# Kernel tuning notes

Measured on AMD Instinct MI355X. Metric: run time of the kernel, lower is better.

The kernel has to match this reference:

```python
import jax, jax.numpy as jnp
import numpy as np
import math

B, S, HID, H, D = 8, 1024, 1024, 16, 64
MAX_POS = 1024  # max_position_embeddings


def setup_inputs() -> dict:
    key = jax.random.key(0)
    ks = jax.random.split(key, 8)
    sc = 1.0 / math.sqrt(HID)
    return {
        "hidden_states": jax.random.normal(ks[0], (B, S, HID), jnp.float32),
        "Wq": jax.random.normal(ks[1], (HID, HID), jnp.float32) * sc,
        "bq": jnp.zeros((HID,), jnp.float32),
        "Wk": jax.random.normal(ks[2], (HID, HID), jnp.float32) * sc,
        "bk": jnp.zeros((HID,), jnp.float32),
        "Wv": jax.random.normal(ks[3], (HID, HID), jnp.float32) * sc,
        "bv": jnp.zeros((HID,), jnp.float32),
        "dist_table": jax.random.normal(ks[4], (2 * MAX_POS - 1, D), jnp.float32) * 0.02,
    }


def _heads(x):
    # [B,S,HID] -> [B,H,S,D]
    return x.reshape(B, S, H, D).transpose(0, 2, 1, 3)


def reference(hidden_states, Wq, bq, Wk, bk, Wv, bv, dist_table):
    q = _heads(hidden_states @ Wq + bq)            # [B,H,S,D]
    k = _heads(hidden_states @ Wk + bk)            # [B,H,S,D]
    # NOTE: source bug — value_layer uses the key projection in self-attention path.
    v = _heads(hidden_states @ Wk + bk)            # [B,H,S,D]

    scores = jnp.einsum("bhld,bhrd->bhlr", q, k)   # [B,H,S,S]

    # relative_key_query positional bias
    pos = jnp.arange(S)
    distance = pos[:, None] - pos[None, :]          # [S,S] in [-(S-1), S-1]
    pos_emb = dist_table[distance + MAX_POS - 1]    # [S,S,D]
    rel_q = jnp.einsum("bhld,lrd->bhlr", q, pos_emb)
    rel_k = jnp.einsum("bhrd,lrd->bhlr", k, pos_emb)
    scores = (scores + rel_q + rel_k) / math.sqrt(D)

    probs = jax.nn.softmax(scores, axis=-1)         # dropout is identity at inference
    ctx = jnp.einsum("bhlr,bhrd->bhld", probs, v)   # [B,H,S,D]
    ctx = ctx.transpose(0, 2, 1, 3).reshape(B, S, HID)
    return ctx
```

## Files before the change

### kernel.cpp

```cpp
#include <hip/hip_runtime.h>
#include <hip/hip_bf16.h>


typedef float  f32x4 __attribute__((ext_vector_type(4)));
typedef short  s16x8 __attribute__((ext_vector_type(8)));
typedef unsigned short u16x4 __attribute__((ext_vector_type(4)));

#define MFMA16(a,b,c) __builtin_amdgcn_mfma_f32_16x16x32_bf16((a),(b),(c),0,0,0)

static __device__ __forceinline__ unsigned short f2b(float x){
    unsigned int u = __float_as_uint(x);
    unsigned int r = (u + 0x7fffu + ((u >> 16) & 1u)) >> 16;
    return (unsigned short)r;
}
static __device__ __forceinline__ float b2f(unsigned short b){
    return __uint_as_float(((unsigned int)b) << 16);
}
static __device__ __forceinline__ void gl_lds16(const unsigned short* g, unsigned short* l){
    __builtin_amdgcn_global_load_lds(
        (const __attribute__((address_space(1))) unsigned int*)g,
        (__attribute__((address_space(3))) unsigned int*)l, 16, 0, 0);
}

__global__ void prep_table(const float* __restrict__ T, unsigned short* __restrict__ Tb){
    int i = blockIdx.x * 256 + threadIdx.x;
    if (i < 2047 * 64)      Tb[i] = f2b(T[i]);
    else if (i < 2048 * 64) Tb[i] = 0;
}

__global__ __launch_bounds__(256)
void prep_a(const float* __restrict__ Hs,
            unsigned short* __restrict__ Ahi, unsigned short* __restrict__ Alo){
    int i = (blockIdx.x * 256 + threadIdx.x) * 8;
    float v[8];
    *(f32x4*)&v[0] = *(const f32x4*)(Hs + i);
    *(f32x4*)&v[4] = *(const f32x4*)(Hs + i + 4);
    unsigned short h8[8] __attribute__((aligned(16)));
    unsigned short l8[8] __attribute__((aligned(16)));
#pragma unroll
    for (int j = 0; j < 8; j++) {
        unsigned short h = f2b(v[j]);
        h8[j] = h;
        l8[j] = f2b(v[j] - b2f(h));
    }
    *(s16x8*)&Ahi[i] = *(s16x8*)h8;
    *(s16x8*)&Alo[i] = *(s16x8*)l8;
}

__global__ __launch_bounds__(256)
void prep_w(const float* __restrict__ Wq, const float* __restrict__ Wk,
            unsigned short* __restrict__ WqThi, unsigned short* __restrict__ WqTlo,
            unsigned short* __restrict__ WkThi, unsigned short* __restrict__ WkTlo){
    __shared__ unsigned short LH[64][72];
    __shared__ unsigned short LL[64][72];
    const int bx = blockIdx.x;
    const float* W = (bx & 1) ? Wk : Wq;
    unsigned short* Thi = (bx & 1) ? WkThi : WqThi;
    unsigned short* Tlo = (bx & 1) ? WkTlo : WqTlo;
    const int tile = bx >> 1;
    const int k0 = (tile >> 4) * 64, n0 = (tile & 15) * 64;
    const int t = threadIdx.x;
    const int r = t >> 3, c8 = (t & 7) * 8;
#pragma unroll
    for (int half = 0; half < 2; half++) {
        int rr = r + half * 32;
        const float* p = W + (size_t)(k0 + rr) * 1024 + n0 + c8;
        float v[8];
        *(f32x4*)&v[0] = *(const f32x4*)p;
        *(f32x4*)&v[4] = *(const f32x4*)(p + 4);
#pragma unroll
        for (int j = 0; j < 8; j++) {
            unsigned short h = f2b(v[j]);
            LH[rr][c8 + j] = h;
            LL[rr][c8 + j] = f2b(v[j] - b2f(h));
        }
    }
    __syncthreads();
    const int n = t >> 2, kg = (t & 3) * 16;
    unsigned short oh[16] __attribute__((aligned(16)));
    unsigned short ol[16] __attribute__((aligned(16)));
#pragma unroll
    for (int j = 0; j < 16; j++) { oh[j] = LH[kg + j][n]; ol[j] = LL[kg + j][n]; }
    unsigned short* dh = Thi + (size_t)(n0 + n) * 1024 + k0 + kg;
    unsigned short* dl = Tlo + (size_t)(n0 + n) * 1024 + k0 + kg;
    *(s16x8*)dh       = *(s16x8*)&oh[0];
    *(s16x8*)(dh + 8) = *(s16x8*)&oh[8];
    *(s16x8*)dl       = *(s16x8*)&ol[0];
    *(s16x8*)(dl + 8) = *(s16x8*)&ol[8];
}

__global__ __launch_bounds__(512, 4)
void proj_gemm(const unsigned short* __restrict__ Ahi, const unsigned short* __restrict__ Alo,
               const unsigned short* __restrict__ WqThi, const unsigned short* __restrict__ WqTlo,
               const unsigned short* __restrict__ WkThi, const unsigned short* __restrict__ WkTlo,
               const float* __restrict__ bq, const float* __restrict__ bk,
               unsigned short* __restrict__ qbf, unsigned short* __restrict__ kbf,
               unsigned short* __restrict__ kTbf)
{
    __shared__ __attribute__((aligned(16))) unsigned short SL[16384];

    const int t = threadIdx.x, lane = t & 63, w = t >> 6;
    const int q4 = lane >> 4, l15 = lane & 15;
    const int wm = w >> 1, wn = w & 1;
    const int ntile = blockIdx.x & 15, mtile = blockIdx.x >> 4;
    const int m0 = mtile * 128, cn0 = (ntile & 7) * 128;
    const unsigned short* Bh = (ntile < 8) ? WqThi : WkThi;
    const unsigned short* Bl = (ntile < 8) ? WqTlo : WkTlo;

    f32x4 acc[2][4];
#pragma unroll
    for (int i = 0; i < 2; i++)
#pragma unroll
        for (int j = 0; j < 4; j++) acc[i][j] = (f32x4){0.f, 0.f, 0.f, 0.f};

    const int lr = lane >> 2, lc = (lane & 3) * 8;

    for (int kk0 = 0; kk0 < 1024; kk0 += 32) {
        __syncthreads();
#pragma unroll
        for (int i = 0; i < 4; i++) {
            const int seg = w * 4 + i;
            const int tid = seg >> 3, row0 = (seg & 7) * 16;
            const unsigned short* g;
            if      (tid == 0) g = Ahi + (size_t)(m0 + row0 + lr) * 1024 + kk0 + lc;
            else if (tid == 1) g = Alo + (size_t)(m0 + row0 + lr) * 1024 + kk0 + lc;
            else if (tid == 2) g = Bh  + (size_t)(cn0 + row0 + lr) * 1024 + kk0 + lc;
            else               g = Bl  + (size_t)(cn0 + row0 + lr) * 1024 + kk0 + lc;
            gl_lds16(g, &SL[seg * 512]);
        }
        __syncthreads();

        s16x8 ah[2], al[2], bh8[4], bl8[4];
#pragma unroll
        for (int sm = 0; sm < 2; sm++) {
            int r = wm * 32 + sm * 16 + l15;
            ah[sm] = *(const s16x8*)&SL[r * 32 + q4 * 8];
            al[sm] = *(const s16x8*)&SL[4096 + r * 32 + q4 * 8];
        }
#pragma unroll
        for (int sn = 0; sn < 4; sn++) {
            int r = wn * 64 + sn * 16 + l15;
            bh8[sn] = *(const s16x8*)&SL[8192 + r * 32 + q4 * 8];
            bl8[sn] = *(const s16x8*)&SL[12288 + r * 32 + q4 * 8];
        }
#pragma unroll
        for (int sm = 0; sm < 2; sm++)
#pragma unroll
            for (int sn = 0; sn < 4; sn++) {
                f32x4 a = acc[sm][sn];
                a = MFMA16(ah[sm], bh8[sn], a);
                a = MFMA16(ah[sm], bl8[sn], a);
                a = MFMA16(al[sm], bh8[sn], a);
                acc[sm][sn] = a;
            }
    }

#pragma unroll
    for (int sm = 0; sm < 2; sm++) {
#pragma unroll
        for (int sn = 0; sn < 4; sn++) {
            const int coln = ntile * 128 + wn * 64 + sn * 16 + l15;
            const float bias = (ntile < 8) ? bq[coln] : bk[coln - 1024];
            const int mbase = m0 + wm * 32 + sm * 16 + q4 * 4;
            const int bb = mbase >> 10, ss0 = mbase & 1023;
            unsigned short vb[4];
#pragma unroll
            for (int reg = 0; reg < 4; reg++) vb[reg] = f2b(acc[sm][sn][reg] + bias);
            if (ntile < 8) {
                const int hh = coln >> 6, d = coln & 63;
#pragma unroll
                for (int reg = 0; reg < 4; reg++)
                    qbf[(((size_t)(bb * 16 + hh) * 1024) + ss0 + reg) * 64 + d] = vb[reg];
            } else {
                const int ck = coln - 1024;
                const int hh = ck >> 6, d = ck & 63;
#pragma unroll
                for (int reg = 0; reg < 4; reg++)
                    kbf[(((size_t)(bb * 16 + hh) * 1024) + ss0 + reg) * 64 + d] = vb[reg];
                u16x4 pk = { vb[0], vb[1], vb[2], vb[3] };
                *(u16x4*)&kTbf[(((size_t)(bb * 16 + hh) * 64) + d) * 1024 + ss0] = pk;
            }
        }
    }
}

__global__ __launch_bounds__(512, 4)
void attn(const unsigned short* __restrict__ qbf, const unsigned short* __restrict__ kbf,
          const unsigned short* __restrict__ kTbf, const unsigned short* __restrict__ Tbf,
          float* __restrict__ out)
{
    __shared__ __attribute__((aligned(16))) unsigned char LDSRAW[65536];
    unsigned short* Klds = (unsigned short*)LDSRAW;
    unsigned short* Tlds = (unsigned short*)(LDSRAW + 8192);
    unsigned int*   GqS  = (unsigned int*)(LDSRAW + 32768);
    unsigned short* Pw   = (unsigned short*)(LDSRAW + 49152);
    float*          Ep   = (float*)LDSRAW;

    const int t = threadIdx.x;
    const int lane = t & 63, w = t >> 6;
    const int q4 = lane >> 4, l15 = lane & 15;
    const int swz8 = (l15 & 7) * 8;
    const int bh = blockIdx.x & 127;
    const int lb = (blockIdx.x >> 7) * 128;
    const int l0w = lb + w * 16;

    const unsigned short* qb = qbf + (size_t)bh * 65536;
    const unsigned short* kb = kbf + (size_t)bh * 65536;
    const unsigned short* kT = kTbf + (size_t)bh * 65536;

    const s16x8 qf0 = *(const s16x8*)(qb + (l0w + l15) * 64 + q4 * 8);
    const s16x8 qf1 = *(const s16x8*)(qb + (l0w + l15) * 64 + 32 + q4 * 8);

    f32x4 pacc[4];
#pragma unroll
    for (int n = 0; n < 4; n++) pacc[n] = (f32x4){0.f, 0.f, 0.f, 0.f};
    float psum = 0.f;

    unsigned int*   GqW = GqS + w * 512;
    unsigned short* PwW = Pw + w * 1024;

    const int s_row = t >> 3;
    const int s_c8  = (t & 7) * 8;
    const int s_swc = s_c8 ^ ((s_row & 7) << 3);

    int r0 = 0;
    int lo = lb + 960;
    s16x8 kv  = *(const s16x8*)(kb + (size_t)(r0 + s_row) * 64 + s_c8);
    s16x8 tv0 = *(const s16x8*)(Tbf + (size_t)(lo + s_row) * 64 + s_c8);
    s16x8 tv1 = *(const s16x8*)(Tbf + (size_t)(lo + s_row + 64) * 64 + s_c8);
    s16x8 tv2 = *(const s16x8*)(Tbf + (size_t)(lo + s_row + 128) * 64 + s_c8);

    for (int c = 0; c < 16; c++) {
        __syncthreads();
        *(s16x8*)&Klds[s_row * 64 + s_swc]         = kv;
        *(s16x8*)&Tlds[s_row * 64 + s_swc]         = tv0;
        *(s16x8*)&Tlds[(s_row + 64) * 64 + s_swc]  = tv1;
        *(s16x8*)&Tlds[(s_row + 128) * 64 + s_swc] = tv2;
        __syncthreads();

        if (c < 15) {
            int r0n = r0 + 64, lon = lo - 64;
            kv  = *(const s16x8*)(kb + (size_t)(r0n + s_row) * 64 + s_c8);
            tv0 = *(const s16x8*)(Tbf + (size_t)(lon + s_row) * 64 + s_c8);
            tv1 = *(const s16x8*)(Tbf + (size_t)(lon + s_row + 64) * 64 + s_c8);
            tv2 = *(const s16x8*)(Tbf + (size_t)(lon + s_row + 128) * 64 + s_c8);
        }

#pragma unroll
        for (int rs = 0; rs < 4; rs++) {
            const int krow = rs * 16 + l15;
            const s16x8 kf0 = *(const s16x8*)&Klds[krow * 64 + ((q4 * 8) ^ swz8)];
            const s16x8 kf1 = *(const s16x8*)&Klds[krow * 64 + ((32 + q4 * 8) ^ swz8)];
            const int c0 = w * 16 - rs * 16 + 48;
            const int j0 = (c0 + l15) * 64, j1 = (c0 + 16 + l15) * 64;
            const s16x8 tf00 = *(const s16x8*)&Tlds[j0 + ((q4 * 8) ^ swz8)];
            const s16x8 tf01 = *(const s16x8*)&Tlds[j0 + ((32 + q4 * 8) ^ swz8)];
            const s16x8 tf10 = *(const s16x8*)&Tlds[j1 + ((q4 * 8) ^ swz8)];
            const s16x8 tf11 = *(const s16x8*)&Tlds[j1 + ((32 + q4 * 8) ^ swz8)];

            f32x4 s = (f32x4){0.f, 0.f, 0.f, 0.f};
            s = MFMA16(kf0, qf0, s);
            s = MFMA16(kf1, qf1, s);

            f32x4 gq0 = (f32x4){0.f,0.f,0.f,0.f}, gq1 = (f32x4){0.f,0.f,0.f,0.f};
            f32x4 hk0 = (f32x4){0.f,0.f,0.f,0.f}, hk1 = (f32x4){0.f,0.f,0.f,0.f};
            gq0 = MFMA16(qf0, tf00, gq0); gq0 = MFMA16(qf1, tf01, gq0);
            gq1 = MFMA16(qf0, tf10, gq1); gq1 = MFMA16(qf1, tf11, gq1);
            hk0 = MFMA16(kf0, tf00, hk0); hk0 = MFMA16(kf1, tf01, hk0);
            hk1 = MFMA16(kf0, tf10, hk1); hk1 = MFMA16(kf1, tf11, hk1);

            unsigned int* G = GqW + (rs & 1) * 256;
#pragma unroll
            for (int reg = 0; reg < 4; reg++) {
                unsigned int pk = (unsigned int)f2b(gq0[reg]) |
                                  ((unsigned int)f2b(gq1[reg]) << 16);
                G[(q4 * 4 + reg) * 16 + l15] = pk;
            }

            const int n4b = l15 - q4 * 4 + 15;
            float pr[4];
#pragma unroll
            for (int reg = 0; reg < 4; reg++) {
                const int n4 = n4b - reg;
                const int srclane = (n4 & 15) | (lane & 48);
                float a0 = __shfl(hk0[reg], srclane);
                float a1 = __shfl(hk1[reg], srclane);
                float relk = (n4 < 16) ? a0 : a1;
                unsigned int g = G[l15 * 16 + (n4 & 15)];
                float b0v = b2f((unsigned short)(g & 0xffffu));
                float b1v = b2f((unsigned short)(g >> 16));
                float relq = (n4 < 16) ? b0v : b1v;
                float sc = (s[reg] + relq + relk) * 0.125f - 4.0f;
                float p = __expf(sc);
                psum += p;
                pr[reg] = p;
            }
            unsigned int u0 = (unsigned int)f2b(pr[0]) | ((unsigned int)f2b(pr[1]) << 16);
            unsigned int u1 = (unsigned int)f2b(pr[2]) | ((unsigned int)f2b(pr[3]) << 16);
            unsigned long long pk2 = (unsigned long long)u0 | ((unsigned long long)u1 << 32);
            *(unsigned long long*)&PwW[l15 * 64 + ((rs * 16 + q4 * 4) ^ swz8)] = pk2;
        }

        const s16x8 pf0 = *(const s16x8*)&PwW[l15 * 64 + ((q4 * 8) ^ swz8)];
        const s16x8 pf1 = *(const s16x8*)&PwW[l15 * 64 + ((32 + q4 * 8) ^ swz8)];
#pragma unroll
        for (int n = 0; n < 4; n++) {
            const unsigned short* vp = kT + (size_t)(n * 16 + l15) * 1024 + r0;
            const s16x8 vf0 = *(const s16x8*)(vp + q4 * 8);
            const s16x8 vf1 = *(const s16x8*)(vp + 32 + q4 * 8);
            pacc[n] = MFMA16(vf0, pf0, pacc[n]);
            pacc[n] = MFMA16(vf1, pf1, pacc[n]);
        }

        r0 += 64;
        lo -= 64;
    }

    psum += __shfl_xor(psum, 16);
    psum += __shfl_xor(psum, 32);
    const float inv = 1.0f / psum;

    __syncthreads();
    float* EpW = Ep + w * 1088;
#pragma unroll
    for (int n = 0; n < 4; n++) {
        f32x4 v = pacc[n];
        v[0] *= inv; v[1] *= inv; v[2] *= inv; v[3] *= inv;
        *(f32x4*)&EpW[l15 * 68 + n * 16 + q4 * 4] = v;
    }
    const int b0 = bh >> 4, hh = bh & 15;
    const int li = lane >> 2, gg = lane & 3;
#pragma unroll
    for (int cc = 0; cc < 4; cc++) {
        f32x4 v = *(const f32x4*)&EpW[li * 68 + gg * 16 + cc * 4];
        *(f32x4*)&out[((size_t)(b0 * 1024 + l0w + li) * 1024) + hh * 64 + gg * 16 + cc * 4] = v;
    }
}

extern "C" void kernel_launch(void* const* d_in, const int* in_sizes, int n_in,
                              void* d_out, int out_size, void* d_ws, size_t ws_size,
                              hipStream_t stream) {
    (void)in_sizes; (void)n_in; (void)out_size; (void)ws_size;
    const float* Hs = (const float*)d_in[0];
    const float* Wq = (const float*)d_in[1];
    const float* bq = (const float*)d_in[2];
    const float* Wk = (const float*)d_in[3];
    const float* bk = (const float*)d_in[4];
    const float* Tt = (const float*)d_in[7];
    float* out = (float*)d_out;

    unsigned short* qbf   = (unsigned short*)d_ws;
    unsigned short* kbf   = qbf  + (size_t)8 * 1024 * 1024;
    unsigned short* kTbf  = kbf  + (size_t)8 * 1024 * 1024;
    unsigned short* Tbf   = kTbf + (size_t)8 * 1024 * 1024;
    unsigned short* Ahi   = Tbf  + (size_t)2048 * 64;
    unsigned short* Alo   = Ahi  + (size_t)8 * 1024 * 1024;
    unsigned short* WqThi = Alo  + (size_t)8 * 1024 * 1024;
    unsigned short* WqTlo = WqThi + (size_t)1024 * 1024;
    unsigned short* WkThi = WqTlo + (size_t)1024 * 1024;
    unsigned short* WkTlo = WkThi + (size_t)1024 * 1024;

    hipLaunchKernelGGL(prep_table, dim3(512), dim3(256), 0, stream, Tt, Tbf);
    hipLaunchKernelGGL(prep_a, dim3(4096), dim3(256), 0, stream, Hs, Ahi, Alo);
    hipLaunchKernelGGL(prep_w, dim3(512), dim3(256), 0, stream,
                       Wq, Wk, WqThi, WqTlo, WkThi, WkTlo);
    hipLaunchKernelGGL(proj_gemm, dim3(1024), dim3(512), 0, stream,
                       Ahi, Alo, WqThi, WqTlo, WkThi, WkTlo, bq, bk, qbf, kbf, kTbf);
    hipLaunchKernelGGL(attn, dim3(1024), dim3(512), 0, stream,
                       qbf, kbf, kTbf, Tbf, out);
}
```

Before: 411.3 us.

## Use ring-buffered table tiles, direct global-to-LDS loads, and packed bf16 conversions

The positional-table tile in LDS becomes a 192-row ring buffer. Each chunk loads only the 64 new table rows and the new K tile, using global_load_lds (direct global-to-LDS) instead of register staging, and one of the two table fragments is carried over from the previous rs step in registers. Value loads are issued at the top of each chunk to hide latency. The rel-q LDS staging is vectorised with a padded stride, the rel-k shuffle is halved by packing both halves into bf16 before shuffling, and conversions use the hardware packed bf16 instruction. This cuts global and LDS traffic and VALU work, but rel-k is now rounded to bf16 before it is added, and correctness depends on the global_load_lds layout matching the XOR swizzle.

```diff
diff --git a/kernel.cpp b/kernel.cpp
--- a/kernel.cpp
+++ b/kernel.cpp
@@ -5,6 +5,7 @@
 typedef float  f32x4 __attribute__((ext_vector_type(4)));
 typedef short  s16x8 __attribute__((ext_vector_type(8)));
 typedef unsigned short u16x4 __attribute__((ext_vector_type(4)));
+typedef unsigned int   u32x4 __attribute__((ext_vector_type(4)));
 
 #define MFMA16(a,b,c) __builtin_amdgcn_mfma_f32_16x16x32_bf16((a),(b),(c),0,0,0)
 
@@ -15,6 +16,15 @@
 }
 static __device__ __forceinline__ float b2f(unsigned short b){
     return __uint_as_float(((unsigned int)b) << 16);
+}
+static __device__ __forceinline__ unsigned int cvtpk(float a, float b){
+#if defined(__has_builtin) && __has_builtin(__builtin_amdgcn_cvt_pk_bf16_f32)
+    typedef __bf16 bf16x2_t __attribute__((ext_vector_type(2)));
+    bf16x2_t v = __builtin_amdgcn_cvt_pk_bf16_f32(a, b);
+    unsigned int u; __builtin_memcpy(&u, &v, 4); return u;
+#else
+    return (unsigned int)f2b(a) | ((unsigned int)f2b(b) << 16);
+#endif
 }
 static __device__ __forceinline__ void gl_lds16(const unsigned short* g, unsigned short* l){
     __builtin_amdgcn_global_load_lds(
@@ -189,11 +199,11 @@
           const unsigned short* __restrict__ kTbf, const unsigned short* __restrict__ Tbf,
           float* __restrict__ out)
 {
-    __shared__ __attribute__((aligned(16))) unsigned char LDSRAW[65536];
+    __shared__ __attribute__((aligned(16))) unsigned char LDSRAW[59392];
     unsigned short* Klds = (unsigned short*)LDSRAW;
     unsigned short* Tlds = (unsigned short*)(LDSRAW + 8192);
     unsigned int*   GqS  = (unsigned int*)(LDSRAW + 32768);
-    unsigned short* Pw   = (unsigned short*)(LDSRAW + 49152);
+    unsigned short* Pw   = (unsigned short*)(LDSRAW + 43008);
     float*          Ep   = (float*)LDSRAW;
 
     const int t = threadIdx.x;
@@ -211,52 +221,56 @@
     const s16x8 qf0 = *(const s16x8*)(qb + (l0w + l15) * 64 + q4 * 8);
     const s16x8 qf1 = *(const s16x8*)(qb + (l0w + l15) * 64 + 32 + q4 * 8);
 
+    const int dj_r = lane >> 3;
+    const int dj_c = ((lane & 7) ^ dj_r) * 8;
+
+#pragma unroll
+    for (int i = 0; i < 4; i++) {
+        const int seg = w * 4 + i;
+        if (seg < 24) {
+            const unsigned short* g = Tbf + (size_t)(lb + 960 + seg * 8 + dj_r) * 64 + dj_c;
+            gl_lds16(g, Tlds + seg * 512);
+        } else {
+            const int s = seg - 24;
+            const unsigned short* g = kb + (size_t)(s * 8 + dj_r) * 64 + dj_c;
+            gl_lds16(g, Klds + s * 512);
+        }
+    }
+    __syncthreads();
+
     f32x4 pacc[4];
 #pragma unroll
     for (int n = 0; n < 4; n++) pacc[n] = (f32x4){0.f, 0.f, 0.f, 0.f};
     float psum = 0.f;
 
-    unsigned int*   GqW = GqS + w * 512;
+    unsigned int*   GqW = GqS + w * 320;
     unsigned short* PwW = Pw + w * 1024;
 
-    const int s_row = t >> 3;
-    const int s_c8  = (t & 7) * 8;
-    const int s_swc = s_c8 ^ ((s_row & 7) << 3);
+    const int pB0 = 64 + w * 16 + l15;
+    s16x8 tb0 = *(const s16x8*)&Tlds[pB0 * 64 + ((q4 * 8) ^ swz8)];
+    s16x8 tb1 = *(const s16x8*)&Tlds[pB0 * 64 + ((32 + q4 * 8) ^ swz8)];
 
     int r0 = 0;
-    int lo = lb + 960;
-    s16x8 kv  = *(const s16x8*)(kb + (size_t)(r0 + s_row) * 64 + s_c8);
-    s16x8 tv0 = *(const s16x8*)(Tbf + (size_t)(lo + s_row) * 64 + s_c8);
-    s16x8 tv1 = *(const s16x8*)(Tbf + (size_t)(lo + s_row + 64) * 64 + s_c8);
-    s16x8 tv2 = *(const s16x8*)(Tbf + (size_t)(lo + s_row + 128) * 64 + s_c8);
-
     for (int c = 0; c < 16; c++) {
-        __syncthreads();
-        *(s16x8*)&Klds[s_row * 64 + s_swc]         = kv;
-        *(s16x8*)&Tlds[s_row * 64 + s_swc]         = tv0;
-        *(s16x8*)&Tlds[(s_row + 64) * 64 + s_swc]  = tv1;
-        *(s16x8*)&Tlds[(s_row + 128) * 64 + s_swc] = tv2;
-        __syncthreads();
-
-        if (c < 15) {
-            int r0n = r0 + 64, lon = lo - 64;
-            kv  = *(const s16x8*)(kb + (size_t)(r0n + s_row) * 64 + s_c8);
-            tv0 = *(const s16x8*)(Tbf + (size_t)(lon + s_row) * 64 + s_c8);
-            tv1 = *(const s16x8*)(Tbf + (size_t)(lon + s_row + 64) * 64 + s_c8);
-            tv2 = *(const s16x8*)(Tbf + (size_t)(lon + s_row + 128) * 64 + s_c8);
-        }
-
+        s16x8 vf[4][2];
+#pragma unroll
+        for (int n = 0; n < 4; n++) {
+            const unsigned short* vp = kT + (size_t)(n * 16 + l15) * 1024 + r0;
+            vf[n][0] = *(const s16x8*)(vp + q4 * 8);
+            vf[n][1] = *(const s16x8*)(vp + 32 + q4 * 8);
+        }
+
+        const int base = 1008 - 64 * c + w * 16;
 #pragma unroll
         for (int rs = 0; rs < 4; rs++) {
             const int krow = rs * 16 + l15;
             const s16x8 kf0 = *(const s16x8*)&Klds[krow * 64 + ((q4 * 8) ^ swz8)];
             const s16x8 kf1 = *(const s16x8*)&Klds[krow * 64 + ((32 + q4 * 8) ^ swz8)];
-            const int c0 = w * 16 - rs * 16 + 48;
-            const int j0 = (c0 + l15) * 64, j1 = (c0 + 16 + l15) * 64;
-            const s16x8 tf00 = *(const s16x8*)&Tlds[j0 + ((q4 * 8) ^ swz8)];
-            const s16x8 tf01 = *(const s16x8*)&Tlds[j0 + ((32 + q4 * 8) ^ swz8)];
-            const s16x8 tf10 = *(const s16x8*)&Tlds[j1 + ((q4 * 8) ^ swz8)];
-            const s16x8 tf11 = *(const s16x8*)&Tlds[j1 + ((32 + q4 * 8) ^ swz8)];
+
+            const int p0 = (base - rs * 16) % 192;
+            int pa = p0 + l15; if (pa >= 192) pa -= 192;
+            const s16x8 ta0 = *(const s16x8*)&Tlds[pa * 64 + ((q4 * 8) ^ swz8)];
+            const s16x8 ta1 = *(const s16x8*)&Tlds[pa * 64 + ((32 + q4 * 8) ^ swz8)];
 
             f32x4 s = (f32x4){0.f, 0.f, 0.f, 0.f};
             s = MFMA16(kf0, qf0, s);
@@ -264,18 +278,15 @@
 
             f32x4 gq0 = (f32x4){0.f,0.f,0.f,0.f}, gq1 = (f32x4){0.f,0.f,0.f,0.f};
             f32x4 hk0 = (f32x4){0.f,0.f,0.f,0.f}, hk1 = (f32x4){0.f,0.f,0.f,0.f};
-            gq0 = MFMA16(qf0, tf00, gq0); gq0 = MFMA16(qf1, tf01, gq0);
-            gq1 = MFMA16(qf0, tf10, gq1); gq1 = MFMA16(qf1, tf11, gq1);
-            hk0 = MFMA16(kf0, tf00, hk0); hk0 = MFMA16(kf1, tf01, hk0);
-            hk1 = MFMA16(kf0, tf10, hk1); hk1 = MFMA16(kf1, tf11, hk1);
-
-            unsigned int* G = GqW + (rs & 1) * 256;
-#pragma unroll
-            for (int reg = 0; reg < 4; reg++) {
-                unsigned int pk = (unsigned int)f2b(gq0[reg]) |
-                                  ((unsigned int)f2b(gq1[reg]) << 16);
-                G[(q4 * 4 + reg) * 16 + l15] = pk;
-            }
+            gq0 = MFMA16(qf0, ta0, gq0); gq0 = MFMA16(qf1, ta1, gq0);
+            gq1 = MFMA16(qf0, tb0, gq1); gq1 = MFMA16(qf1, tb1, gq1);
+            hk0 = MFMA16(kf0, ta0, hk0); hk0 = MFMA16(kf1, ta1, hk0);
+            hk1 = MFMA16(kf0, tb0, hk1); hk1 = MFMA16(kf1, tb1, hk1);
+
+            u32x4 gpk;
+#pragma unroll
+            for (int reg = 0; reg < 4; reg++) gpk[reg] = cvtpk(gq0[reg], gq1[reg]);
+            *(u32x4*)&GqW[l15 * 20 + q4 * 4] = gpk;
 
             const int n4b = l15 - q4 * 4 + 15;
             float pr[4];
@@ -283,37 +294,47 @@
             for (int reg = 0; reg < 4; reg++) {
                 const int n4 = n4b - reg;
                 const int srclane = (n4 & 15) | (lane & 48);
-                float a0 = __shfl(hk0[reg], srclane);
-                float a1 = __shfl(hk1[reg], srclane);
-                float relk = (n4 < 16) ? a0 : a1;
-                unsigned int g = G[l15 * 16 + (n4 & 15)];
-                float b0v = b2f((unsigned short)(g & 0xffffu));
-                float b1v = b2f((unsigned short)(g >> 16));
-                float relq = (n4 < 16) ? b0v : b1v;
-                float sc = (s[reg] + relq + relk) * 0.125f - 4.0f;
+                const unsigned int hpk = cvtpk(hk0[reg], hk1[reg]);
+                const unsigned int gsh = (unsigned int)__shfl((int)hpk, srclane);
+                const unsigned int rkb = (n4 < 16) ? (gsh << 16) : (gsh & 0xffff0000u);
+                const unsigned int gq  = GqW[(n4 & 15) * 20 + l15];
+                const unsigned int rqb = (n4 < 16) ? (gq << 16) : (gq & 0xffff0000u);
+                float sc = (s[reg] + __uint_as_float(rqb) + __uint_as_float(rkb)) * 0.125f - 4.0f;
                 float p = __expf(sc);
                 psum += p;
                 pr[reg] = p;
             }
-            unsigned int u0 = (unsigned int)f2b(pr[0]) | ((unsigned int)f2b(pr[1]) << 16);
-            unsigned int u1 = (unsigned int)f2b(pr[2]) | ((unsigned int)f2b(pr[3]) << 16);
+            unsigned int u0 = cvtpk(pr[0], pr[1]);
+            unsigned int u1 = cvtpk(pr[2], pr[3]);
             unsigned long long pk2 = (unsigned long long)u0 | ((unsigned long long)u1 << 32);
             *(unsigned long long*)&PwW[l15 * 64 + ((rs * 16 + q4 * 4) ^ swz8)] = pk2;
+
+            tb0 = ta0; tb1 = ta1;
         }
 
         const s16x8 pf0 = *(const s16x8*)&PwW[l15 * 64 + ((q4 * 8) ^ swz8)];
         const s16x8 pf1 = *(const s16x8*)&PwW[l15 * 64 + ((32 + q4 * 8) ^ swz8)];
 #pragma unroll
         for (int n = 0; n < 4; n++) {
-            const unsigned short* vp = kT + (size_t)(n * 16 + l15) * 1024 + r0;
-            const s16x8 vf0 = *(const s16x8*)(vp + q4 * 8);
-            const s16x8 vf1 = *(const s16x8*)(vp + 32 + q4 * 8);
-            pacc[n] = MFMA16(vf0, pf0, pacc[n]);
-            pacc[n] = MFMA16(vf1, pf1, pacc[n]);
-        }
-
+            pacc[n] = MFMA16(vf[n][0], pf0, pacc[n]);
+            pacc[n] = MFMA16(vf[n][1], pf1, pacc[n]);
+        }
+
+        if (c < 15) {
+            __syncthreads();
+            const int cn = c + 1;
+            {
+                const unsigned short* g = kb + (size_t)(cn * 64 + w * 8 + dj_r) * 64 + dj_c;
+                gl_lds16(g, Klds + w * 512);
+            }
+            {
+                const int pnew = (1152 - 64 * cn) % 192;
+                const unsigned short* g = Tbf + (size_t)(lb + 960 - 64 * cn + w * 8 + dj_r) * 64 + dj_c;
+                gl_lds16(g, Tlds + pnew * 64 + w * 512);
+            }
+            __syncthreads();
+        }
         r0 += 64;
-        lo -= 64;
     }
 
     psum += __shfl_xor(psum, 16);
```

Result: faster. 392.3 us (-4.6%).
